# Kernel tuning notes

Hardware: AMD Instinct MI355X
Metric: run time of the kernel (lower is better)

## Reference

```python
import jax, jax.numpy as jnp
import numpy as np

L, H, P_LOC = 32768, 512, 256  # seq len, in/out dim, local state dim (conj_sym: P//2)
DT_MIN, DT_MAX = 1e-3, 1e-1
STEP_RESCALE = 1.0


def setup_inputs() -> dict:
    key = jax.random.key(0)
    ks = jax.random.split(key, 10)
    # stable eigenvalues: negative real part (mimics HiPPO init real part -1/2)
    Lambda_re = -0.1 - jax.random.uniform(ks[0], (P_LOC,), dtype=jnp.float32)
    Lambda_im = jax.random.normal(ks[1], (P_LOC,), dtype=jnp.float32) * jnp.pi
    B_re = jax.random.normal(ks[2], (P_LOC, H), dtype=jnp.float32) / jnp.sqrt(2.0 * H)
    B_im = jax.random.normal(ks[3], (P_LOC, H), dtype=jnp.float32) / jnp.sqrt(2.0 * H)
    C_re = jax.random.normal(ks[4], (H, P_LOC), dtype=jnp.float32) / jnp.sqrt(2.0 * P_LOC)
    C_im = jax.random.normal(ks[5], (H, P_LOC), dtype=jnp.float32) / jnp.sqrt(2.0 * P_LOC)
    D = jax.random.normal(ks[6], (H,), dtype=jnp.float32)
    u01 = jax.random.uniform(ks[7], (P_LOC,), dtype=jnp.float32)
    log_step = u01 * (jnp.log(DT_MAX) - jnp.log(DT_MIN)) + jnp.log(DT_MIN)
    input_sequence = jax.random.normal(ks[8], (L, H), dtype=jnp.float32)
    integration_timesteps = jax.random.uniform(ks[9], (L,), dtype=jnp.float32)
    return {
        "input_sequence": input_sequence,
        "integration_timesteps": integration_timesteps,
        "Lambda_re": Lambda_re, "Lambda_im": Lambda_im,
        "B_re": B_re, "B_im": B_im,
        "C_re": C_re, "C_im": C_im,
        "D": D, "log_step": log_step,
    }


def _binop(q_i, q_j):
    A_i, b_i = q_i
    A_j, b_j = q_j
    return (A_j * A_i, A_j * b_i + b_j)


def reference(input_sequence, integration_timesteps, Lambda_re, Lambda_im,
              B_re, B_im, C_re, C_im, D, log_step):
    Lambda = Lambda_re + 1j * Lambda_im          # (P,)
    B = B_re + 1j * B_im                         # (P, H)
    C_tilde = C_re + 1j * C_im                   # (H, P)
    step = STEP_RESCALE * jnp.exp(log_step)      # (P,)
    # ZOH discretization per timestep: Delta[l,p] = step[p] * dt[l]
    Delta = integration_timesteps[:, None] * step[None, :]          # (L, P)
    Lambda_bar = jnp.exp(Lambda[None, :] * Delta)                   # (L, P) complex
    gamma_bar = (Lambda_bar - 1.0) / Lambda[None, :]                # (L, P) complex
    Bu = gamma_bar * jnp.einsum("lh,ph->lp", input_sequence.astype(B.dtype), B)
    _, xs = jax.lax.associative_scan(_binop, (Lambda_bar, Bu))      # (L, P)
    # conj_sym=True -> output is 2 * Re(C x)
    ys = 2.0 * jnp.einsum("lp,hp->lh", xs, C_tilde).real            # (L, H)
    return ys + D[None, :] * input_sequence
```

## Files before the change

kernel.cpp:

```cpp
#include <hip/hip_runtime.h>
#include <math.h>

#define L_SEQ 32768
#define H_DIM 512
#define P_DIM 256
#define K_DIM 512
#define CHUNK 32
#define NCHUNK (L_SEQ / CHUNK)

typedef __bf16 bf16x8 __attribute__((ext_vector_type(8)));
typedef __bf16 bf16x4 __attribute__((ext_vector_type(4)));
typedef float floatx4 __attribute__((ext_vector_type(4)));

__device__ __forceinline__ void gll16(const void* g, void* l) {
    __builtin_amdgcn_global_load_lds(
        (__attribute__((address_space(1))) void*)(g),
        (__attribute__((address_space(3))) void*)(l), 16, 0, 0);
}

__global__ __launch_bounds__(256) void f2bf_kernel(
    const float* __restrict__ in, __bf16* __restrict__ out)
{
    const int i = blockIdx.x * 256 + threadIdx.x;
    float4 v = ((const float4*)in)[i];
    bf16x4 o;
    o.x = (__bf16)v.x; o.y = (__bf16)v.y; o.z = (__bf16)v.z; o.w = (__bf16)v.w;
    ((bf16x4*)out)[i] = o;
}

__global__ __launch_bounds__(256) void build_c2_kernel(
    const float* __restrict__ Cre, const float* __restrict__ Cim,
    __bf16* __restrict__ C2)
{
    const int h = blockIdx.x;
    const int p = threadIdx.x;
    C2[h * 512 + p]       = (__bf16)Cre[h * P_DIM + p];
    C2[h * 512 + 256 + p] = (__bf16)(-Cim[h * P_DIM + p]);
}

template <int EPI>
__global__ __launch_bounds__(256) void mfma_gemm_kernel(
    const __bf16* __restrict__ A,
    const __bf16* __restrict__ Bm,
    float* __restrict__ Out,
    const float* __restrict__ U,
    const float* __restrict__ Dv)
{
    __shared__ __bf16 As[128 * 32];
    __shared__ __bf16 Bs[128 * 32];

    const int tid = threadIdx.x;
    const int w  = tid >> 6;
    const int ln = tid & 63;
    const int bm = blockIdx.x;
    const int bn = blockIdx.y;

    floatx4 acc[4][4];
    #pragma unroll
    for (int i = 0; i < 4; ++i)
        #pragma unroll
        for (int j = 0; j < 4; ++j)
            acc[i][j] = (floatx4){0.f, 0.f, 0.f, 0.f};

    const int lr = ln >> 2;
    const int lce = (ln & 3) << 3;
    const size_t arow = (size_t)(bm * 128 + w * 16 + lr) * K_DIM;
    const size_t brow = (size_t)(bn * 128 + w * 16 + lr) * K_DIM;

    __bf16* lA0 = As + w * 512;
    __bf16* lA1 = As + 2048 + w * 512;
    __bf16* lB0 = Bs + w * 512;
    __bf16* lB1 = Bs + 2048 + w * 512;

    const int wm = (w >> 1) * 64;
    const int wn = (w & 1) * 64;
    const int fr = ln & 15;
    const int fq = (ln >> 4) * 8;

    for (int kt = 0; kt < K_DIM; kt += 32) {
        __syncthreads();
        gll16(A  + arow + kt + lce,                      lA0);
        gll16(A  + arow + (size_t)64 * K_DIM + kt + lce, lA1);
        gll16(Bm + brow + kt + lce,                      lB0);
        gll16(Bm + brow + (size_t)64 * K_DIM + kt + lce, lB1);
        __syncthreads();

        bf16x8 a[4], b[4];
        #pragma unroll
        for (int mt = 0; mt < 4; ++mt)
            a[mt] = *(bf16x8*)&As[(wm + mt * 16 + fr) * 32 + fq];
        #pragma unroll
        for (int nt = 0; nt < 4; ++nt)
            b[nt] = *(bf16x8*)&Bs[(wn + nt * 16 + fr) * 32 + fq];

        #pragma unroll
        for (int mt = 0; mt < 4; ++mt)
            #pragma unroll
            for (int nt = 0; nt < 4; ++nt)
                acc[mt][nt] = __builtin_amdgcn_mfma_f32_16x16x32_bf16(
                    a[mt], b[nt], acc[mt][nt], 0, 0, 0);
    }

    const int rq = (ln >> 4) * 4;
    #pragma unroll
    for (int mt = 0; mt < 4; ++mt) {
        const int gro = bm * 128 + wm + mt * 16 + rq;
        #pragma unroll
        for (int nt = 0; nt < 4; ++nt) {
            const int gco = bn * 128 + wn + nt * 16 + (ln & 15);
            float dh = (EPI == 1) ? Dv[gco] : 0.f;
            #pragma unroll
            for (int r = 0; r < 4; ++r) {
                const size_t o = (size_t)(gro + r) * 512 + gco;
                if (EPI == 0) {
                    Out[o] = acc[mt][nt][r];
                } else {
                    Out[o] = 2.0f * acc[mt][nt][r] + dh * U[o];
                }
            }
        }
    }
}

template <int WRITE_X>
__global__ __launch_bounds__(256) void scan_chunk_kernel(
    const float* __restrict__ dts,
    const float* __restrict__ Lre_g, const float* __restrict__ Lim_g,
    const float* __restrict__ logstep,
    const float* __restrict__ G2,
    __bf16* __restrict__ X2,
    float4* __restrict__ Agg,
    const float2* __restrict__ Carry)
{
    const int p = threadIdx.x;
    const int c = blockIdx.x;

    const float lre = Lre_g[p];
    const float lim = Lim_g[p];
    const float stp = __expf(logstep[p]);
    const float inv_den = 1.0f / (lre * lre + lim * lim);

    float Are = 1.0f, Aim = 0.0f;
    float xre, xim;
    if (WRITE_X) {
        float2 cc = Carry[c * P_DIM + p];
        xre = cc.x; xim = cc.y;
    } else {
        xre = 0.0f; xim = 0.0f;
    }

    const int base = c * CHUNK;
    for (int i = 0; i < CHUNK; ++i) {
        const int l = base + i;
        const float d = stp * dts[l];
        const float er = __expf(lre * d);
        float sn, cs;
        __sincosf(lim * d, &sn, &cs);
        const float are = er * cs;
        const float aim = er * sn;
        const float am1 = are - 1.0f;
        const float gr = (am1 * lre + aim * lim) * inv_den;
        const float gi = (aim * lre - am1 * lim) * inv_den;

        const size_t idx = (size_t)l * 512 + p;
        const float ure = G2[idx];
        const float uim = G2[idx + 256];
        const float bre = gr * ure - gi * uim;
        const float bim = gr * uim + gi * ure;

        const float nxre = are * xre - aim * xim + bre;
        const float nxim = are * xim + aim * xre + bim;
        xre = nxre; xim = nxim;

        if (WRITE_X) {
            X2[idx]       = (__bf16)xre;
            X2[idx + 256] = (__bf16)xim;
        } else {
            const float nAre = are * Are - aim * Aim;
            const float nAim = are * Aim + aim * Are;
            Are = nAre; Aim = nAim;
        }
    }

    if (!WRITE_X) {
        Agg[p * NCHUNK + c] = make_float4(Are, Aim, xre, xim);
    }
}

__global__ __launch_bounds__(1024) void carry_kernel(
    const float4* __restrict__ Agg,
    float2* __restrict__ Carry)
{
    const int p = blockIdx.x;
    const int c = threadIdx.x;

    __shared__ float sAr[NCHUNK], sAi[NCHUNK], sBr[NCHUNK], sBi[NCHUNK];

    float4 v = Agg[p * NCHUNK + c];
    float ar = v.x, ai = v.y, br = v.z, bi = v.w;
    sAr[c] = ar; sAi[c] = ai; sBr[c] = br; sBi[c] = bi;
    __syncthreads();

    #pragma unroll
    for (int off = 1; off < NCHUNK; off <<= 1) {
        float par, pai, pbr, pbi;
        const bool act = (c >= off);
        if (act) {
            par = sAr[c - off]; pai = sAi[c - off];
            pbr = sBr[c - off]; pbi = sBi[c - off];
        }
        __syncthreads();
        if (act) {
            const float nbr = ar * pbr - ai * pbi + br;
            const float nbi = ar * pbi + ai * pbr + bi;
            const float nar = ar * par - ai * pai;
            const float nai = ar * pai + ai * par;
            ar = nar; ai = nai; br = nbr; bi = nbi;
            sAr[c] = ar; sAi[c] = ai; sBr[c] = br; sBi[c] = bi;
        }
        __syncthreads();
    }

    float cr = 0.0f, ci = 0.0f;
    if (c > 0) { cr = sBr[c - 1]; ci = sBi[c - 1]; }
    Carry[c * P_DIM + p] = make_float2(cr, ci);
}

extern "C" void kernel_launch(void* const* d_in, const int* in_sizes, int n_in,
                              void* d_out, int out_size, void* d_ws, size_t ws_size,
                              hipStream_t stream) {
    const float* U       = (const float*)d_in[0];
    const float* dts     = (const float*)d_in[1];
    const float* Lre     = (const float*)d_in[2];
    const float* Lim     = (const float*)d_in[3];
    const float* Bre     = (const float*)d_in[4];
    const float* Bim     = (const float*)d_in[5];
    const float* Cre     = (const float*)d_in[6];
    const float* Cim     = (const float*)d_in[7];
    const float* Dv      = (const float*)d_in[8];
    const float* logstep = (const float*)d_in[9];
    float* out = (float*)d_out;

    char* ws = (char*)d_ws;
    __bf16* Ubf  = (__bf16*)ws;
    __bf16* X2   = Ubf;
    __bf16* B2   = (__bf16*)(ws + (size_t)L_SEQ * 512 * 2);
    __bf16* C2   = B2 + 512 * 512;
    float4* Agg  = (float4*)(C2 + 512 * 512);
    float2* Carry = (float2*)(Agg + (size_t)P_DIM * NCHUNK);

    float* G2 = out;

    f2bf_kernel<<<(L_SEQ * H_DIM) / 4 / 256, 256, 0, stream>>>(U, Ubf);
    f2bf_kernel<<<(P_DIM * H_DIM) / 4 / 256, 256, 0, stream>>>(Bre, B2);
    f2bf_kernel<<<(P_DIM * H_DIM) / 4 / 256, 256, 0, stream>>>(Bim, B2 + P_DIM * H_DIM);
    build_c2_kernel<<<H_DIM, 256, 0, stream>>>(Cre, Cim, C2);

    dim3 g1(L_SEQ / 128, 4);
    mfma_gemm_kernel<0><<<g1, 256, 0, stream>>>(Ubf, B2, G2, nullptr, nullptr);

    scan_chunk_kernel<0><<<NCHUNK, 256, 0, stream>>>(
        dts, Lre, Lim, logstep, G2, nullptr, Agg, nullptr);
    carry_kernel<<<P_DIM, NCHUNK, 0, stream>>>(Agg, Carry);
    scan_chunk_kernel<1><<<NCHUNK, 256, 0, stream>>>(
        dts, Lre, Lim, logstep, G2, X2, nullptr, Carry);

    dim3 g2(L_SEQ / 128, 4);
    mfma_gemm_kernel<1><<<g2, 256, 0, stream>>>(X2, C2, out, U, Dv);
}
```

Before: 244.4 us.

## Fuse input bf16 conversion into GEMM1 and store interleaved bf16 intermediates

Removes the separate fp32-to-bf16 conversion pass over the input by having the first GEMM load fp32 tiles into LDS and convert them in registers. The projected input G2 is now stored as interleaved bf16 re/im pairs in workspace instead of fp32 in the output buffer. The scan reads and writes each pair as one 32-bit word in place, and prefetches a whole chunk into registers. B2 and C2 are rebuilt with interleaved rows/columns to match. This cuts global memory traffic across the GEMM-scan-GEMM pipeline, at the cost of extra rounding of G2 to bf16 and a larger fp32 A tile in LDS.

```diff
diff --git a/kernel.cpp b/kernel.cpp
--- a/kernel.cpp
+++ b/kernel.cpp
@@ -9,7 +9,6 @@
 #define NCHUNK (L_SEQ / CHUNK)
 
 typedef __bf16 bf16x8 __attribute__((ext_vector_type(8)));
-typedef __bf16 bf16x4 __attribute__((ext_vector_type(4)));
 typedef float floatx4 __attribute__((ext_vector_type(4)));
 
 __device__ __forceinline__ void gll16(const void* g, void* l) {
@@ -18,14 +17,14 @@
         (__attribute__((address_space(3))) void*)(l), 16, 0, 0);
 }
 
-__global__ __launch_bounds__(256) void f2bf_kernel(
-    const float* __restrict__ in, __bf16* __restrict__ out)
-{
-    const int i = blockIdx.x * 256 + threadIdx.x;
-    float4 v = ((const float4*)in)[i];
-    bf16x4 o;
-    o.x = (__bf16)v.x; o.y = (__bf16)v.y; o.z = (__bf16)v.z; o.w = (__bf16)v.w;
-    ((bf16x4*)out)[i] = o;
+__global__ __launch_bounds__(512) void build_b2_kernel(
+    const float* __restrict__ Bre, const float* __restrict__ Bim,
+    __bf16* __restrict__ B2)
+{
+    const int p = blockIdx.x;
+    const int h = threadIdx.x;
+    B2[(2 * p) * 512 + h]     = (__bf16)Bre[p * H_DIM + h];
+    B2[(2 * p + 1) * 512 + h] = (__bf16)Bim[p * H_DIM + h];
 }
 
 __global__ __launch_bounds__(256) void build_c2_kernel(
@@ -34,12 +33,99 @@
 {
     const int h = blockIdx.x;
     const int p = threadIdx.x;
-    C2[h * 512 + p]       = (__bf16)Cre[h * P_DIM + p];
-    C2[h * 512 + 256 + p] = (__bf16)(-Cim[h * P_DIM + p]);
-}
-
-template <int EPI>
-__global__ __launch_bounds__(256) void mfma_gemm_kernel(
+    C2[h * 512 + 2 * p]     = (__bf16)Cre[h * P_DIM + p];
+    C2[h * 512 + 2 * p + 1] = (__bf16)(-Cim[h * P_DIM + p]);
+}
+
+__global__ __launch_bounds__(256) void gemm1_kernel(
+    const float* __restrict__ A,
+    const __bf16* __restrict__ Bm,
+    __bf16* __restrict__ Out)
+{
+    __shared__ float  Asf[128 * 32];
+    __shared__ __bf16 Bs [128 * 32];
+
+    const int tid = threadIdx.x;
+    const int w  = tid >> 6;
+    const int ln = tid & 63;
+    const int bm = blockIdx.x;
+    const int bn = blockIdx.y;
+
+    floatx4 acc[4][4];
+    #pragma unroll
+    for (int i = 0; i < 4; ++i)
+        #pragma unroll
+        for (int j = 0; j < 4; ++j)
+            acc[i][j] = (floatx4){0.f, 0.f, 0.f, 0.f};
+
+    const int a_r = ln >> 3;
+    const int a_c = (ln & 7) << 2;
+    const int b_r = ln >> 2;
+    const int b_c = (ln & 3) << 3;
+    const size_t brow = (size_t)(bn * 128 + w * 16 + b_r) * K_DIM;
+
+    float*  lA[4];
+    size_t  gAr[4];
+    #pragma unroll
+    for (int q = 0; q < 4; ++q) {
+        lA[q] = Asf + (q * 32 + w * 8) * 32;
+        gAr[q] = (size_t)(bm * 128 + q * 32 + w * 8 + a_r) * K_DIM;
+    }
+    __bf16* lB0 = Bs + w * 512;
+    __bf16* lB1 = Bs + 2048 + w * 512;
+
+    const int wm = (w >> 1) * 64;
+    const int wn = (w & 1) * 64;
+    const int fr = ln & 15;
+    const int fq = (ln >> 4) * 8;
+
+    for (int kt = 0; kt < K_DIM; kt += 32) {
+        __syncthreads();
+        #pragma unroll
+        for (int q = 0; q < 4; ++q)
+            gll16(A + gAr[q] + kt + a_c, lA[q]);
+        gll16(Bm + brow + kt + b_c,                      lB0);
+        gll16(Bm + brow + (size_t)64 * K_DIM + kt + b_c, lB1);
+        __syncthreads();
+
+        bf16x8 a[4], b[4];
+        #pragma unroll
+        for (int mt = 0; mt < 4; ++mt) {
+            floatx4 a0 = *(floatx4*)&Asf[(wm + mt * 16 + fr) * 32 + fq];
+            floatx4 a1 = *(floatx4*)&Asf[(wm + mt * 16 + fr) * 32 + fq + 4];
+            #pragma unroll
+            for (int r = 0; r < 4; ++r) {
+                a[mt][r]     = (__bf16)a0[r];
+                a[mt][4 + r] = (__bf16)a1[r];
+            }
+        }
+        #pragma unroll
+        for (int nt = 0; nt < 4; ++nt)
+            b[nt] = *(bf16x8*)&Bs[(wn + nt * 16 + fr) * 32 + fq];
+
+        #pragma unroll
+        for (int mt = 0; mt < 4; ++mt)
+            #pragma unroll
+            for (int nt = 0; nt < 4; ++nt)
+                acc[mt][nt] = __builtin_amdgcn_mfma_f32_16x16x32_bf16(
+                    a[mt], b[nt], acc[mt][nt], 0, 0, 0);
+    }
+
+    const int rq = (ln >> 4) * 4;
+    #pragma unroll
+    for (int mt = 0; mt < 4; ++mt) {
+        const int gro = bm * 128 + wm + mt * 16 + rq;
+        #pragma unroll
+        for (int nt = 0; nt < 4; ++nt) {
+            const int gco = bn * 128 + wn + nt * 16 + (ln & 15);
+            #pragma unroll
+            for (int r = 0; r < 4; ++r)
+                Out[(size_t)(gro + r) * 512 + gco] = (__bf16)acc[mt][nt][r];
+        }
+    }
+}
+
+__global__ __launch_bounds__(256) void gemm2_kernel(
     const __bf16* __restrict__ A,
     const __bf16* __restrict__ Bm,
     float* __restrict__ Out,
@@ -108,15 +194,11 @@
         #pragma unroll
         for (int nt = 0; nt < 4; ++nt) {
             const int gco = bn * 128 + wn + nt * 16 + (ln & 15);
-            float dh = (EPI == 1) ? Dv[gco] : 0.f;
+            const float dh = Dv[gco];
             #pragma unroll
             for (int r = 0; r < 4; ++r) {
                 const size_t o = (size_t)(gro + r) * 512 + gco;
-                if (EPI == 0) {
-                    Out[o] = acc[mt][nt][r];
-                } else {
-                    Out[o] = 2.0f * acc[mt][nt][r] + dh * U[o];
-                }
+                Out[o] = 2.0f * acc[mt][nt][r] + dh * U[o];
             }
         }
     }
@@ -127,13 +209,22 @@
     const float* __restrict__ dts,
     const float* __restrict__ Lre_g, const float* __restrict__ Lim_g,
     const float* __restrict__ logstep,
-    const float* __restrict__ G2,
-    __bf16* __restrict__ X2,
+    unsigned int* __restrict__ G2u,
     float4* __restrict__ Agg,
     const float2* __restrict__ Carry)
 {
     const int p = threadIdx.x;
     const int c = blockIdx.x;
+    const int base = c * CHUNK;
+
+    unsigned int g[CHUNK];
+    float dt[CHUNK];
+    #pragma unroll
+    for (int i = 0; i < CHUNK; ++i)
+        g[i] = G2u[(size_t)(base + i) * 256 + p];
+    #pragma unroll
+    for (int i = 0; i < CHUNK; ++i)
+        dt[i] = dts[base + i];
 
     const float lre = Lre_g[p];
     const float lim = Lim_g[p];
@@ -149,10 +240,9 @@
         xre = 0.0f; xim = 0.0f;
     }
 
-    const int base = c * CHUNK;
+    #pragma unroll
     for (int i = 0; i < CHUNK; ++i) {
-        const int l = base + i;
-        const float d = stp * dts[l];
+        const float d = stp * dt[i];
         const float er = __expf(lre * d);
         float sn, cs;
         __sincosf(lim * d, &sn, &cs);
@@ -162,9 +252,8 @@
         const float gr = (am1 * lre + aim * lim) * inv_den;
         const float gi = (aim * lre - am1 * lim) * inv_den;
 
-        const size_t idx = (size_t)l * 512 + p;
-        const float ure = G2[idx];
-        const float uim = G2[idx + 256];
+        const float ure = __uint_as_float(g[i] << 16);
+        const float uim = __uint_as_float(g[i] & 0xffff0000u);
         const float bre = gr * ure - gi * uim;
         const float bim = gr * uim + gi * ure;
 
@@ -173,8 +262,11 @@
         xre = nxre; xim = nxim;
 
         if (WRITE_X) {
-            X2[idx]       = (__bf16)xre;
-            X2[idx + 256] = (__bf16)xim;
+            __bf16 xr = (__bf16)xre;
+            __bf16 xi = (__bf16)xim;
+            unsigned int o = (unsigned int)*(unsigned short*)&xr |
+                             ((unsigned int)*(unsigned short*)&xi << 16);
+            G2u[(size_t)(base + i) * 256 + p] = o;
         } else {
             const float nAre = are * Are - aim * Aim;
             const float nAim = are * Aim + aim * Are;
@@ -182,9 +274,8 @@
         }
     }
 
-    if (!WRITE_X) {
+    if (!WRITE_X)
         Agg[p * NCHUNK + c] = make_float4(Are, Aim, xre, xim);
-    }
 }
 
 __global__ __launch_bounds__(1024) void carry_kernel(
@@ -242,29 +333,25 @@
     float* out = (float*)d_out;
 
     char* ws = (char*)d_ws;
-    __bf16* Ubf  = (__bf16*)ws;
-    __bf16* X2   = Ubf;
-    __bf16* B2   = (__bf16*)(ws + (size_t)L_SEQ * 512 * 2);
-    __bf16* C2   = B2 + 512 * 512;
-    float4* Agg  = (float4*)(C2 + 512 * 512);
+    __bf16* G2 = (__bf16*)ws;
+    __bf16* B2 = (__bf16*)(ws + (size_t)L_SEQ * 512 * 2);
+    __bf16* C2 = B2 + 512 * 512;
+    float4* Agg = (float4*)(C2 + 512 * 512);
     float2* Carry = (float2*)(Agg + (size_t)P_DIM * NCHUNK);
 
-    float* G2 = out;
-
-    f2bf_kernel<<<(L_SEQ * H_DIM) / 4 / 256, 256, 0, stream>>>(U, Ubf);
-    f2bf_kernel<<<(P_DIM * H_DIM) / 4 / 256, 256, 0, stream>>>(Bre, B2);
-    f2bf_kernel<<<(P_DIM * H_DIM) / 4 / 256, 256, 0, stream>>>(Bim, B2 + P_DIM * H_DIM);
+    build_b2_kernel<<<P_DIM, 512, 0, stream>>>(Bre, Bim, B2);
     build_c2_kernel<<<H_DIM, 256, 0, stream>>>(Cre, Cim, C2);
 
     dim3 g1(L_SEQ / 128, 4);
-    mfma_gemm_kernel<0><<<g1, 256, 0, stream>>>(Ubf, B2, G2, nullptr, nullptr);
-
+    gemm1_kernel<<<g1, 256, 0, stream>>>(U, B2, G2);
+
+    unsigned int* G2u = (unsigned int*)G2;
     scan_chunk_kernel<0><<<NCHUNK, 256, 0, stream>>>(
-        dts, Lre, Lim, logstep, G2, nullptr, Agg, nullptr);
+        dts, Lre, Lim, logstep, G2u, Agg, nullptr);
     carry_kernel<<<P_DIM, NCHUNK, 0, stream>>>(Agg, Carry);
     scan_chunk_kernel<1><<<NCHUNK, 256, 0, stream>>>(
-        dts, Lre, Lim, logstep, G2, X2, nullptr, Carry);
+        dts, Lre, Lim, logstep, G2u, nullptr, Carry);
 
     dim3 g2(L_SEQ / 128, 4);
-    mfma_gemm_kernel<1><<<g2, 256, 0, stream>>>(X2, C2, out, U, Dv);
-}
+    gemm2_kernel<<<g2, 256, 0, stream>>>(G2, C2, out, U, Dv);
+}
```

New measurement: 232.2 us. 1.05x faster.
